# Kernel optimization log

Measured on AMD Instinct MI355X. Metric: run time of the kernel, lower is better.

The kernel has to match this reference:

```python
import jax, jax.numpy as jnp
import numpy as np

B, S, H, I, E = 2, 1024, 1024, 4096, 8

def setup_inputs() -> dict:
    key = jax.random.key(0)
    ks = jax.random.split(key, 8)
    s_h = 1.0 / np.sqrt(H)
    s_i = 1.0 / np.sqrt(I)
    return {
        "x": jax.random.normal(ks[0], (B, S, H), dtype=jnp.float32),
        "router_w": jax.random.uniform(ks[1], (H, E), jnp.float32, -s_h, s_h),
        "router_b": jax.random.uniform(ks[2], (E,), jnp.float32, -s_h, s_h),
        "w1": jax.random.uniform(ks[3], (E, H, I), jnp.float32, -s_h, s_h),
        "b1": jax.random.uniform(ks[4], (E, I), jnp.float32, -s_h, s_h),
        "w2": jax.random.uniform(ks[5], (E, I, H), jnp.float32, -s_i, s_i),
        "b2": jax.random.uniform(ks[6], (E, H), jnp.float32, -s_i, s_i),
        "game_emb": jax.random.normal(ks[7], (E, H), dtype=jnp.float32) * 0.02,
    }

def reference(x, router_w, router_b, w1, b1, w2, b2, game_emb):
    # Router: top-1 expert per token (softmax is monotone, argmax of logits)
    logits = jnp.einsum('bsh,he->bse', x, router_w) + router_b  # [B,S,E]
    expert_idx = jnp.argmax(logits, axis=-1)                    # [B,S] int
    out = jnp.zeros_like(x)
    n_experts = w1.shape[0]
    for e in range(n_experts):  # fixed small expert loop
        mask = (expert_idx == e)[..., None]                     # [B,S,1]
        sel = x + 0.1 * game_emb[e]                             # embedding add
        h = jax.nn.gelu(jnp.einsum('bsh,hi->bsi', sel, w1[e]) + b1[e], approximate=False)
        y = jnp.einsum('bsi,ih->bsh', h, w2[e]) + b2[e]
        out = jnp.where(mask, y, out)                           # scatter combine
    return out
```

## Files before the change

kernel.cpp:

```cpp
#include <hip/hip_runtime.h>
#include <hip/hip_bf16.h>
#include <math.h>

#define HDIM 1024
#define IDIM 4096
#define NE 8
#define NTOK 2048
#define PADROWS 256

typedef __attribute__((ext_vector_type(8))) short bf16x8;
typedef __attribute__((ext_vector_type(4))) float f32x4;

__device__ __forceinline__ unsigned int f2bf(float f) {
    unsigned int u = __float_as_uint(f);
    u = (u + 0x7FFFu + ((u >> 16) & 1u)) >> 16;
    return u;
}

__device__ __forceinline__ unsigned int pkbf2(float lo, float hi) {
    union { __hip_bfloat162 h; unsigned int u; } cv;
    cv.h = __float22bfloat162_rn(make_float2(lo, hi));
    return cv.u;
}

__device__ __forceinline__ float comp4(const float4& v, int c) {
    return c == 0 ? v.x : c == 1 ? v.y : c == 2 ? v.z : v.w;
}

__device__ __forceinline__ int swz8(int i) { return (i ^ (i >> 3)) & 7; }

__device__ __forceinline__ float gelu_erf(float v) {
    float x = v * 0.70710678118654752f;
    float ax = fabsf(x);
    float t = 1.0f / (1.0f + 0.3275911f * ax);
    float p = t * (0.254829592f + t * (-0.284496736f + t * (1.421413741f +
              t * (-1.453152027f + t * 1.061405429f))));
    float er = 1.0f - p * __expf(-x * x);
    er = copysignf(er, v);
    return 0.5f * v * (1.0f + er);
}

template<typename T, typename U>
__device__ __forceinline__ void gld16(const T* g, U* l) {
    __builtin_amdgcn_global_load_lds((const __attribute__((address_space(1))) void*)g,
                                     (__attribute__((address_space(3))) void*)l, 16, 0, 0);
}

__global__ __launch_bounds__(256) void router_k(const float* __restrict__ x,
                                                const float* __restrict__ rw,
                                                const float* __restrict__ rb,
                                                int* __restrict__ eidx,
                                                int* __restrict__ counts) {
    const int wave = threadIdx.x >> 6, lane = threadIdx.x & 63;
    const int t = blockIdx.x * 4 + wave;
    if (t >= NTOK) return;
    double acc[NE];
#pragma unroll
    for (int e = 0; e < NE; e++) acc[e] = 0.0;
    for (int h = lane; h < HDIM; h += 64) {
        double xv = (double)x[(size_t)t * HDIM + h];
        const float4* rwp = (const float4*)&rw[h * NE];
        float4 r0 = rwp[0], r1 = rwp[1];
        acc[0] += xv * (double)r0.x;  acc[1] += xv * (double)r0.y;
        acc[2] += xv * (double)r0.z;  acc[3] += xv * (double)r0.w;
        acc[4] += xv * (double)r1.x;  acc[5] += xv * (double)r1.y;
        acc[6] += xv * (double)r1.z;  acc[7] += xv * (double)r1.w;
    }
#pragma unroll
    for (int m = 32; m >= 1; m >>= 1) {
#pragma unroll
        for (int e = 0; e < NE; e++) acc[e] += __shfl_xor(acc[e], m);
    }
    if (lane == 0) {
        double best = acc[0] + (double)rb[0];
        int be = 0;
#pragma unroll
        for (int e = 1; e < NE; e++) {
            double v = acc[e] + (double)rb[e];
            if (v > best) { best = v; be = e; }
        }
        eidx[t] = be;
        atomicAdd(&counts[be], 1);
    }
}

__global__ void scan_k(const int* __restrict__ counts, int* __restrict__ offsets) {
    if (threadIdx.x == 0 && blockIdx.x == 0) {
        int s = 0;
        for (int e = 0; e < NE; e++) { offsets[e] = s; s += counts[e]; }
        offsets[NE] = s;
    }
}

__global__ __launch_bounds__(256) void gather_k(const float* __restrict__ x,
                                                const float* __restrict__ gemb,
                                                const int* __restrict__ eidx,
                                                const int* __restrict__ offsets,
                                                int* __restrict__ cursors,
                                                int* __restrict__ rowmap,
                                                unsigned short* __restrict__ Xg) {
    __shared__ int srow, se;
    const int t = blockIdx.x;
    if (threadIdx.x == 0) {
        int e = eidx[t];
        int pos = atomicAdd(&cursors[e], 1);
        int row = offsets[e] + pos;
        rowmap[row] = t;
        srow = row; se = e;
    }
    __syncthreads();
    const int row = srow, e = se;
    const int c = threadIdx.x * 4;
    float4 xv = *(const float4*)&x[(size_t)t * HDIM + c];
    float4 gv = *(const float4*)&gemb[(size_t)e * HDIM + c];
    ushort4 o;
    o.x = (unsigned short)f2bf(xv.x + 0.1f * gv.x);
    o.y = (unsigned short)f2bf(xv.y + 0.1f * gv.y);
    o.z = (unsigned short)f2bf(xv.z + 0.1f * gv.z);
    o.w = (unsigned short)f2bf(xv.w + 0.1f * gv.w);
    *(ushort4*)&Xg[(size_t)row * HDIM + c] = o;
}

template<int EPI>
__global__ __launch_bounds__(512, 2) void moe_gemm_k(
        const unsigned short* __restrict__ A, int lda, int Kfull, int ksplit,
        const float* __restrict__ Bw, int ldbN,
        const float* __restrict__ bias,
        const int* __restrict__ offsets, const int* __restrict__ rowmap,
        unsigned short* __restrict__ Hout, float* __restrict__ Yout,
        float* __restrict__ P, size_t pstride) {
    __shared__ __align__(16) unsigned short At[2][256 * 64];
    __shared__ __align__(16) unsigned short Bt[128 * 64];

    const int e = blockIdx.z & 7;
    const int split = blockIdx.z >> 3;
    const int rend = offsets[e + 1];
    const int r0 = offsets[e] + blockIdx.y * 256;
    if (r0 >= rend) return;
    const int c0 = blockIdx.x * 128;
    const int kbeg = split * ksplit;
    const int nt = ksplit / 64;
    const float* Be = Bw + (size_t)e * Kfull * ldbN;

    const int tid = threadIdx.x;
    const int wave = tid >> 6, lane = tid & 63;
    const int wr = (wave >> 1) * 64, wc = (wave & 1) * 64;
    const int l15 = lane & 15, l4 = lane >> 4;

    const int cg = tid & 31, kid = tid >> 5;
    const int bcol = cg * 4;
    const int boct = kid >> 1, bhalf = kid & 1;
    const float* bsrc = Be + (size_t)(kid * 4) * ldbN + c0 + bcol;
    int bwo[4];
#pragma unroll
    for (int i = 0; i < 4; ++i) {
        int col = bcol + i;
        bwo[i] = col * 64 + (boct ^ swz8(col)) * 8 + bhalf * 4;
    }

    const unsigned short* adsrc[4];
    int adoff[4];
#pragma unroll
    for (int p = 0; p < 4; ++p) {
        int gidx = p * 512 + tid;
        int row = gidx >> 3, ps = gidx & 7;
        adsrc[p] = A + (size_t)(r0 + row) * lda + (ps ^ swz8(row)) * 8;
        adoff[p] = gidx * 8;
    }

    float4 fv[4];
    auto loadB = [&](int kabs) {
#pragma unroll
        for (int j = 0; j < 4; ++j)
            fv[j] = *(const float4*)&bsrc[(size_t)(kabs + j) * ldbN];
    };
    auto dmaA = [&](int kabs, int buf) {
#pragma unroll
        for (int p = 0; p < 4; ++p)
            gld16(adsrc[p] + kabs, &At[buf][adoff[p]]);
    };

    f32x4 acc[4][4];
#pragma unroll
    for (int m = 0; m < 4; ++m)
#pragma unroll
        for (int n = 0; n < 4; ++n) acc[m][n] = (f32x4){0.f, 0.f, 0.f, 0.f};

    loadB(kbeg);
    dmaA(kbeg, 0);
    for (int t = 0; t < nt; ++t) {
        const int cur = t & 1;
#pragma unroll
        for (int i = 0; i < 4; ++i) {
            uint2 w;
            w.x = pkbf2(comp4(fv[0], i), comp4(fv[1], i));
            w.y = pkbf2(comp4(fv[2], i), comp4(fv[3], i));
            *(uint2*)&Bt[bwo[i]] = w;
        }
        if (t + 1 < nt) {
            loadB(kbeg + (t + 1) * 64);
            dmaA(kbeg + (t + 1) * 64, cur ^ 1);
            asm volatile("s_waitcnt vmcnt(8) lgkmcnt(0)" ::: "memory");
        } else {
            asm volatile("s_waitcnt vmcnt(0) lgkmcnt(0)" ::: "memory");
        }
        __builtin_amdgcn_s_barrier();
        __builtin_amdgcn_sched_barrier(0);
#pragma unroll
        for (int kh = 0; kh < 2; ++kh) {
            const int kb = kh * 4 + l4;
            bf16x8 af[4], bfr[4];
#pragma unroll
            for (int m = 0; m < 4; ++m) {
                int row = wr + m * 16 + l15;
                af[m] = *(const bf16x8*)&At[cur][row * 64 + (kb ^ swz8(row)) * 8];
            }
#pragma unroll
            for (int n = 0; n < 4; ++n) {
                int col = wc + n * 16 + l15;
                bfr[n] = *(const bf16x8*)&Bt[col * 64 + (kb ^ swz8(col)) * 8];
            }
#pragma unroll
            for (int m = 0; m < 4; ++m)
#pragma unroll
                for (int n = 0; n < 4; ++n)
                    acc[m][n] = __builtin_amdgcn_mfma_f32_16x16x32_bf16(af[m], bfr[n], acc[m][n], 0, 0, 0);
        }
        __builtin_amdgcn_sched_barrier(0);
        __builtin_amdgcn_s_barrier();
        __builtin_amdgcn_sched_barrier(0);
    }

#pragma unroll
    for (int m = 0; m < 4; ++m) {
#pragma unroll
        for (int r = 0; r < 4; ++r) {
            const int row = r0 + wr + m * 16 + l4 * 4 + r;
            if (row < rend) {
                if constexpr (EPI == 0) {
#pragma unroll
                    for (int n = 0; n < 4; ++n) {
                        int col = c0 + wc + n * 16 + l15;
                        float v = acc[m][n][r] + bias[(size_t)e * ldbN + col];
                        Hout[(size_t)row * IDIM + col] = (unsigned short)f2bf(gelu_erf(v));
                    }
                } else if (split == 0) {
                    const int tt = rowmap[row];
#pragma unroll
                    for (int n = 0; n < 4; ++n) {
                        int col = c0 + wc + n * 16 + l15;
                        Yout[(size_t)tt * HDIM + col] = acc[m][n][r] + bias[(size_t)e * ldbN + col];
                    }
                } else {
                    float* Ps = P + (size_t)(split - 1) * pstride;
#pragma unroll
                    for (int n = 0; n < 4; ++n) {
                        int col = c0 + wc + n * 16 + l15;
                        Ps[(size_t)row * HDIM + col] = acc[m][n][r];
                    }
                }
            }
        }
    }
}

__global__ __launch_bounds__(256) void reduce_k(const float* __restrict__ P,
                                                size_t pstride, int nparts,
                                                const int* __restrict__ rowmap,
                                                float* __restrict__ out) {
    const int row = blockIdx.x;
    const int t = rowmap[row];
    const int c = threadIdx.x * 4;
    f32x4 s = *(const f32x4*)&out[(size_t)t * HDIM + c];
    for (int p = 0; p < nparts; ++p)
        s += *(const f32x4*)&P[(size_t)p * pstride + (size_t)row * HDIM + c];
    *(f32x4*)&out[(size_t)t * HDIM + c] = s;
}

extern "C" void kernel_launch(void* const* d_in, const int* in_sizes, int n_in,
                              void* d_out, int out_size, void* d_ws, size_t ws_size,
                              hipStream_t stream) {
    const float* x    = (const float*)d_in[0];
    const float* rw   = (const float*)d_in[1];
    const float* rb   = (const float*)d_in[2];
    const float* w1   = (const float*)d_in[3];
    const float* b1   = (const float*)d_in[4];
    const float* w2   = (const float*)d_in[5];
    const float* b2   = (const float*)d_in[6];
    const float* gemb = (const float*)d_in[7];
    float* out = (float*)d_out;

    char* ws = (char*)d_ws;
    int* meta    = (int*)ws;
    int* counts  = meta;
    int* cursors = meta + 8;
    int* offsets = meta + 16;
    int* eidx    = meta + 32;
    int* rowmap  = meta + 32 + NTOK;
    size_t off = 32768;
    unsigned short* Xg = (unsigned short*)(ws + off);
    off += (size_t)(NTOK + PADROWS) * HDIM * 2;
    unsigned short* Hbuf = (unsigned short*)(ws + off);
    off += (size_t)(NTOK + PADROWS) * IDIM * 2;
    float* P = (float*)(ws + off);
    const size_t pstride = (size_t)NTOK * HDIM;
    int nsplit = 1;
    if (ws_size >= off + 3 * pstride * 4) nsplit = 4;
    else if (ws_size >= off + 1 * pstride * 4) nsplit = 2;

    hipMemsetAsync(counts, 0, 16 * sizeof(int), stream);
    router_k<<<NTOK / 4, 256, 0, stream>>>(x, rw, rb, eidx, counts);
    scan_k<<<1, 64, 0, stream>>>(counts, offsets);
    gather_k<<<NTOK, 256, 0, stream>>>(x, gemb, eidx, offsets, cursors, rowmap, Xg);
    moe_gemm_k<0><<<dim3(IDIM / 128, 3, NE), 512, 0, stream>>>(
        Xg, HDIM, HDIM, HDIM, w1, IDIM, b1, offsets, rowmap, Hbuf, nullptr, nullptr, 0);
    moe_gemm_k<1><<<dim3(HDIM / 128, 3, NE * nsplit), 512, 0, stream>>>(
        Hbuf, IDIM, IDIM, IDIM / nsplit, w2, HDIM, b2, offsets, rowmap, nullptr, out, P, pstride);
    if (nsplit > 1)
        reduce_k<<<NTOK, 256, 0, stream>>>(P, pstride, nsplit - 1, rowmap, out);
}
```

Before: 228.3 us.

## Retile expert GEMM to 1024-thread blocks with double-buffered B, single A

```diff
diff --git a/kernel.cpp b/kernel.cpp
--- a/kernel.cpp
+++ b/kernel.cpp
@@ -122,85 +122,88 @@
 }
 
 template<int EPI>
-__global__ __launch_bounds__(512, 2) void moe_gemm_k(
+__global__ __launch_bounds__(1024, 4) void moe_gemm_k(
         const unsigned short* __restrict__ A, int lda, int Kfull, int ksplit,
         const float* __restrict__ Bw, int ldbN,
         const float* __restrict__ bias,
         const int* __restrict__ offsets, const int* __restrict__ rowmap,
         unsigned short* __restrict__ Hout, float* __restrict__ Yout,
-        float* __restrict__ P, size_t pstride) {
-    __shared__ __align__(16) unsigned short At[2][256 * 64];
-    __shared__ __align__(16) unsigned short Bt[128 * 64];
-
-    const int e = blockIdx.z & 7;
-    const int split = blockIdx.z >> 3;
+        float* __restrict__ P, size_t pstride, int ncb, int nsp) {
+    __shared__ __align__(16) unsigned short At[256 * 64];
+    __shared__ __align__(16) unsigned short Bt[2][128 * 64];
+
+    const int bid = blockIdx.x;
+    const int e = bid & 7;
+    int loc = bid >> 3;
+    const int cblk = loc % ncb;  loc /= ncb;
+    const int split = loc % nsp;
+    const int yblk = loc / nsp;
+
     const int rend = offsets[e + 1];
-    const int r0 = offsets[e] + blockIdx.y * 256;
+    const int r0 = offsets[e] + yblk * 256;
     if (r0 >= rend) return;
-    const int c0 = blockIdx.x * 128;
+    const int c0 = cblk * 128;
     const int kbeg = split * ksplit;
     const int nt = ksplit / 64;
     const float* Be = Bw + (size_t)e * Kfull * ldbN;
 
     const int tid = threadIdx.x;
     const int wave = tid >> 6, lane = tid & 63;
-    const int wr = (wave >> 1) * 64, wc = (wave & 1) * 64;
+    const int wr = (wave >> 2) * 64;
+    const int wc = (wave & 3) * 32;
     const int l15 = lane & 15, l4 = lane >> 4;
 
     const int cg = tid & 31, kid = tid >> 5;
     const int bcol = cg * 4;
-    const int boct = kid >> 1, bhalf = kid & 1;
-    const float* bsrc = Be + (size_t)(kid * 4) * ldbN + c0 + bcol;
+    const int boct = kid >> 2;
+    const int brow = (kid * 2) & 7;
+    const float* bsrc = Be + (size_t)(kid * 2) * ldbN + c0 + bcol;
     int bwo[4];
 #pragma unroll
     for (int i = 0; i < 4; ++i) {
         int col = bcol + i;
-        bwo[i] = col * 64 + (boct ^ swz8(col)) * 8 + bhalf * 4;
-    }
-
-    const unsigned short* adsrc[4];
-    int adoff[4];
-#pragma unroll
-    for (int p = 0; p < 4; ++p) {
-        int gidx = p * 512 + tid;
+        bwo[i] = col * 64 + (boct ^ swz8(col)) * 8 + brow;
+    }
+
+    const unsigned short* adsrc[2];
+    int adoff[2];
+#pragma unroll
+    for (int p = 0; p < 2; ++p) {
+        int gidx = p * 1024 + tid;
         int row = gidx >> 3, ps = gidx & 7;
         adsrc[p] = A + (size_t)(r0 + row) * lda + (ps ^ swz8(row)) * 8;
         adoff[p] = gidx * 8;
     }
 
-    float4 fv[4];
+    float4 fv[2];
     auto loadB = [&](int kabs) {
 #pragma unroll
-        for (int j = 0; j < 4; ++j)
+        for (int j = 0; j < 2; ++j)
             fv[j] = *(const float4*)&bsrc[(size_t)(kabs + j) * ldbN];
     };
-    auto dmaA = [&](int kabs, int buf) {
-#pragma unroll
-        for (int p = 0; p < 4; ++p)
-            gld16(adsrc[p] + kabs, &At[buf][adoff[p]]);
+    auto dmaA = [&](int kabs) {
+#pragma unroll
+        for (int p = 0; p < 2; ++p)
+            gld16(adsrc[p] + kabs, &At[adoff[p]]);
     };
 
-    f32x4 acc[4][4];
+    f32x4 acc[4][2];
 #pragma unroll
     for (int m = 0; m < 4; ++m)
 #pragma unroll
-        for (int n = 0; n < 4; ++n) acc[m][n] = (f32x4){0.f, 0.f, 0.f, 0.f};
+        for (int n = 0; n < 2; ++n) acc[m][n] = (f32x4){0.f, 0.f, 0.f, 0.f};
 
     loadB(kbeg);
-    dmaA(kbeg, 0);
+    dmaA(kbeg);
     for (int t = 0; t < nt; ++t) {
         const int cur = t & 1;
-#pragma unroll
-        for (int i = 0; i < 4; ++i) {
-            uint2 w;
-            w.x = pkbf2(comp4(fv[0], i), comp4(fv[1], i));
-            w.y = pkbf2(comp4(fv[2], i), comp4(fv[3], i));
-            *(uint2*)&Bt[bwo[i]] = w;
-        }
+        if (t > 0) dmaA(kbeg + t * 64);
+#pragma unroll
+        for (int i = 0; i < 4; ++i)
+            *(unsigned int*)&Bt[cur][bwo[i]] = pkbf2(comp4(fv[0], i), comp4(fv[1], i));
         if (t + 1 < nt) {
             loadB(kbeg + (t + 1) * 64);
-            dmaA(kbeg + (t + 1) * 64, cur ^ 1);
-            asm volatile("s_waitcnt vmcnt(8) lgkmcnt(0)" ::: "memory");
+            asm volatile("s_waitcnt vmcnt(2) lgkmcnt(0)" ::: "memory");
         } else {
             asm volatile("s_waitcnt vmcnt(0) lgkmcnt(0)" ::: "memory");
         }
@@ -209,21 +212,21 @@
 #pragma unroll
         for (int kh = 0; kh < 2; ++kh) {
             const int kb = kh * 4 + l4;
-            bf16x8 af[4], bfr[4];
+            bf16x8 af[4], bfr[2];
 #pragma unroll
             for (int m = 0; m < 4; ++m) {
                 int row = wr + m * 16 + l15;
-                af[m] = *(const bf16x8*)&At[cur][row * 64 + (kb ^ swz8(row)) * 8];
+                af[m] = *(const bf16x8*)&At[row * 64 + (kb ^ swz8(row)) * 8];
             }
 #pragma unroll
-            for (int n = 0; n < 4; ++n) {
+            for (int n = 0; n < 2; ++n) {
                 int col = wc + n * 16 + l15;
-                bfr[n] = *(const bf16x8*)&Bt[col * 64 + (kb ^ swz8(col)) * 8];
+                bfr[n] = *(const bf16x8*)&Bt[cur][col * 64 + (kb ^ swz8(col)) * 8];
             }
 #pragma unroll
             for (int m = 0; m < 4; ++m)
 #pragma unroll
-                for (int n = 0; n < 4; ++n)
+                for (int n = 0; n < 2; ++n)
                     acc[m][n] = __builtin_amdgcn_mfma_f32_16x16x32_bf16(af[m], bfr[n], acc[m][n], 0, 0, 0);
         }
         __builtin_amdgcn_sched_barrier(0);
@@ -239,7 +242,7 @@
             if (row < rend) {
                 if constexpr (EPI == 0) {
 #pragma unroll
-                    for (int n = 0; n < 4; ++n) {
+                    for (int n = 0; n < 2; ++n) {
                         int col = c0 + wc + n * 16 + l15;
                         float v = acc[m][n][r] + bias[(size_t)e * ldbN + col];
                         Hout[(size_t)row * IDIM + col] = (unsigned short)f2bf(gelu_erf(v));
@@ -247,14 +250,14 @@
                 } else if (split == 0) {
                     const int tt = rowmap[row];
 #pragma unroll
-                    for (int n = 0; n < 4; ++n) {
+                    for (int n = 0; n < 2; ++n) {
                         int col = c0 + wc + n * 16 + l15;
                         Yout[(size_t)tt * HDIM + col] = acc[m][n][r] + bias[(size_t)e * ldbN + col];
                     }
                 } else {
                     float* Ps = P + (size_t)(split - 1) * pstride;
 #pragma unroll
-                    for (int n = 0; n < 4; ++n) {
+                    for (int n = 0; n < 2; ++n) {
                         int col = c0 + wc + n * 16 + l15;
                         Ps[(size_t)row * HDIM + col] = acc[m][n][r];
                     }
@@ -312,10 +315,12 @@
     router_k<<<NTOK / 4, 256, 0, stream>>>(x, rw, rb, eidx, counts);
     scan_k<<<1, 64, 0, stream>>>(counts, offsets);
     gather_k<<<NTOK, 256, 0, stream>>>(x, gemb, eidx, offsets, cursors, rowmap, Xg);
-    moe_gemm_k<0><<<dim3(IDIM / 128, 3, NE), 512, 0, stream>>>(
-        Xg, HDIM, HDIM, HDIM, w1, IDIM, b1, offsets, rowmap, Hbuf, nullptr, nullptr, 0);
-    moe_gemm_k<1><<<dim3(HDIM / 128, 3, NE * nsplit), 512, 0, stream>>>(
-        Hbuf, IDIM, IDIM, IDIM / nsplit, w2, HDIM, b2, offsets, rowmap, nullptr, out, P, pstride);
+    moe_gemm_k<0><<<512, 1024, 0, stream>>>(
+        Xg, HDIM, HDIM, HDIM, w1, IDIM, b1, offsets, rowmap,
+        Hbuf, nullptr, nullptr, 0, 32, 1);
+    moe_gemm_k<1><<<128 * nsplit, 1024, 0, stream>>>(
+        Hbuf, IDIM, IDIM, IDIM / nsplit, w2, HDIM, b2, offsets, rowmap,
+        nullptr, out, P, pstride, 8, nsplit);
     if (nsplit > 1)
         reduce_k<<<NTOK, 256, 0, stream>>>(P, pstride, nsplit - 1, rowmap, out);
 }
```

New measurement: 210.0 us. 8.0% less time.

## Split-K the first MoE GEMM with a fused GELU combine; flatten and interleave grids

Applied to the files above, without the earlier changes.

```diff
diff --git a/kernel.cpp b/kernel.cpp
--- a/kernel.cpp
+++ b/kernel.cpp
@@ -122,40 +122,47 @@
 }
 
 template<int EPI>
-__global__ __launch_bounds__(512, 2) void moe_gemm_k(
+__global__ __launch_bounds__(512, 4) void moe_gemm_k(
         const unsigned short* __restrict__ A, int lda, int Kfull, int ksplit,
         const float* __restrict__ Bw, int ldbN,
         const float* __restrict__ bias,
         const int* __restrict__ offsets, const int* __restrict__ rowmap,
         unsigned short* __restrict__ Hout, float* __restrict__ Yout,
-        float* __restrict__ P, size_t pstride) {
+        float* __restrict__ Pdst, size_t pstride, int ncb, int nsp) {
     __shared__ __align__(16) unsigned short At[2][256 * 64];
     __shared__ __align__(16) unsigned short Bt[128 * 64];
 
-    const int e = blockIdx.z & 7;
-    const int split = blockIdx.z >> 3;
+    const int bid = blockIdx.x;
+    const int e = bid & 7;
+    int loc = bid >> 3;
+    const int cblk = loc % ncb;  loc /= ncb;
+    const int split = loc % nsp;
+    const int yblk = loc / nsp;
+
     const int rend = offsets[e + 1];
-    const int r0 = offsets[e] + blockIdx.y * 256;
+    const int r0 = offsets[e] + yblk * 256;
     if (r0 >= rend) return;
-    const int c0 = blockIdx.x * 128;
+    const int c0 = cblk * 128;
     const int kbeg = split * ksplit;
     const int nt = ksplit / 64;
     const float* Be = Bw + (size_t)e * Kfull * ldbN;
 
     const int tid = threadIdx.x;
     const int wave = tid >> 6, lane = tid & 63;
-    const int wr = (wave >> 1) * 64, wc = (wave & 1) * 64;
+    const int wr = (wave >> 1) * 64;
+    const int wc = (wave & 1) * 64;
     const int l15 = lane & 15, l4 = lane >> 4;
 
-    const int cg = tid & 31, kid = tid >> 5;
+    const int cg = tid & 31, kg = tid >> 5;
     const int bcol = cg * 4;
-    const int boct = kid >> 1, bhalf = kid & 1;
-    const float* bsrc = Be + (size_t)(kid * 4) * ldbN + c0 + bcol;
+    const int boct = kg >> 1;
+    const int bpos = (kg * 4) & 7;
+    const float* bsrc = Be + (size_t)(kg * 4) * ldbN + c0 + bcol;
     int bwo[4];
 #pragma unroll
     for (int i = 0; i < 4; ++i) {
         int col = bcol + i;
-        bwo[i] = col * 64 + (boct ^ swz8(col)) * 8 + bhalf * 4;
+        bwo[i] = col * 64 + ((boct ^ swz8(col)) << 3) + bpos;
     }
 
     const unsigned short* adsrc[4];
@@ -237,14 +244,14 @@
         for (int r = 0; r < 4; ++r) {
             const int row = r0 + wr + m * 16 + l4 * 4 + r;
             if (row < rend) {
-                if constexpr (EPI == 0) {
+                if constexpr (EPI == 2) {
 #pragma unroll
                     for (int n = 0; n < 4; ++n) {
                         int col = c0 + wc + n * 16 + l15;
                         float v = acc[m][n][r] + bias[(size_t)e * ldbN + col];
                         Hout[(size_t)row * IDIM + col] = (unsigned short)f2bf(gelu_erf(v));
                     }
-                } else if (split == 0) {
+                } else if (EPI == 1 && split == 0) {
                     const int tt = rowmap[row];
 #pragma unroll
                     for (int n = 0; n < 4; ++n) {
@@ -252,15 +259,42 @@
                         Yout[(size_t)tt * HDIM + col] = acc[m][n][r] + bias[(size_t)e * ldbN + col];
                     }
                 } else {
-                    float* Ps = P + (size_t)(split - 1) * pstride;
+                    const int slot = (EPI == 1) ? split - 1 : split;
+                    float* Ps = Pdst + (size_t)slot * pstride;
 #pragma unroll
                     for (int n = 0; n < 4; ++n) {
                         int col = c0 + wc + n * 16 + l15;
-                        Ps[(size_t)row * HDIM + col] = acc[m][n][r];
+                        Ps[(size_t)row * ldbN + col] = acc[m][n][r];
                     }
                 }
             }
         }
+    }
+}
+
+__global__ __launch_bounds__(256) void gelu_combine_k(const float* __restrict__ H0,
+                                                      const float* __restrict__ P1,
+                                                      const float* __restrict__ b1,
+                                                      const int* __restrict__ offsets,
+                                                      unsigned short* __restrict__ Hbuf) {
+    const int row = blockIdx.x;
+    int e = 0;
+#pragma unroll
+    for (int i = 1; i < NE; ++i) e += (row >= offsets[i]);
+    const float* bp = b1 + (size_t)e * IDIM;
+    const size_t base = (size_t)row * IDIM;
+#pragma unroll
+    for (int it = 0; it < 4; ++it) {
+        int c = it * 1024 + threadIdx.x * 4;
+        f32x4 a = *(const f32x4*)&H0[base + c];
+        f32x4 b = *(const f32x4*)&P1[base + c];
+        f32x4 bb = *(const f32x4*)&bp[c];
+        ushort4 o;
+        o.x = (unsigned short)f2bf(gelu_erf(a[0] + b[0] + bb[0]));
+        o.y = (unsigned short)f2bf(gelu_erf(a[1] + b[1] + bb[1]));
+        o.z = (unsigned short)f2bf(gelu_erf(a[2] + b[2] + bb[2]));
+        o.w = (unsigned short)f2bf(gelu_erf(a[3] + b[3] + bb[3]));
+        *(ushort4*)&Hbuf[base + c] = o;
     }
 }
 
@@ -302,20 +336,39 @@
     off += (size_t)(NTOK + PADROWS) * HDIM * 2;
     unsigned short* Hbuf = (unsigned short*)(ws + off);
     off += (size_t)(NTOK + PADROWS) * IDIM * 2;
-    float* P = (float*)(ws + off);
-    const size_t pstride = (size_t)NTOK * HDIM;
-    int nsplit = 1;
-    if (ws_size >= off + 3 * pstride * 4) nsplit = 4;
-    else if (ws_size >= off + 1 * pstride * 4) nsplit = 2;
+
+    const size_t f1elems = (size_t)NTOK * IDIM;
+    float* Hraw = nullptr;
+    if (ws_size >= off + 2 * f1elems * 4) {
+        Hraw = (float*)(ws + off);
+        off += 2 * f1elems * 4;
+    }
+    float* P2 = (float*)(ws + off);
+    const size_t ps2 = (size_t)NTOK * HDIM;
+    size_t rem = (ws_size > off) ? ws_size - off : 0;
+    int nsp2 = 1;
+    if (rem >= 7 * ps2 * 4) nsp2 = 8;
+    else if (rem >= 3 * ps2 * 4) nsp2 = 4;
+    else if (rem >= 1 * ps2 * 4) nsp2 = 2;
 
     hipMemsetAsync(counts, 0, 16 * sizeof(int), stream);
     router_k<<<NTOK / 4, 256, 0, stream>>>(x, rw, rb, eidx, counts);
     scan_k<<<1, 64, 0, stream>>>(counts, offsets);
     gather_k<<<NTOK, 256, 0, stream>>>(x, gemb, eidx, offsets, cursors, rowmap, Xg);
-    moe_gemm_k<0><<<dim3(IDIM / 128, 3, NE), 512, 0, stream>>>(
-        Xg, HDIM, HDIM, HDIM, w1, IDIM, b1, offsets, rowmap, Hbuf, nullptr, nullptr, 0);
-    moe_gemm_k<1><<<dim3(HDIM / 128, 3, NE * nsplit), 512, 0, stream>>>(
-        Hbuf, IDIM, IDIM, IDIM / nsplit, w2, HDIM, b2, offsets, rowmap, nullptr, out, P, pstride);
-    if (nsplit > 1)
-        reduce_k<<<NTOK, 256, 0, stream>>>(P, pstride, nsplit - 1, rowmap, out);
-}
+
+    if (Hraw) {
+        moe_gemm_k<0><<<8 * 32 * 2 * 2, 512, 0, stream>>>(
+            Xg, HDIM, HDIM, HDIM / 2, w1, IDIM, b1, offsets, rowmap,
+            nullptr, nullptr, Hraw, f1elems, 32, 2);
+        gelu_combine_k<<<NTOK, 256, 0, stream>>>(Hraw, Hraw + f1elems, b1, offsets, Hbuf);
+    } else {
+        moe_gemm_k<2><<<8 * 32 * 1 * 2, 512, 0, stream>>>(
+            Xg, HDIM, HDIM, HDIM, w1, IDIM, b1, offsets, rowmap,
+            Hbuf, nullptr, nullptr, 0, 32, 1);
+    }
+    moe_gemm_k<1><<<8 * 8 * nsp2 * 2, 512, 0, stream>>>(
+        Hbuf, IDIM, IDIM, IDIM / nsp2, w2, HDIM, b2, offsets, rowmap,
+        nullptr, out, P2, ps2, 8, nsp2);
+    if (nsp2 > 1)
+        reduce_k<<<NTOK, 256, 0, stream>>>(P2, ps2, nsp2 - 1, rowmap, out);
+}
```

Result: slower. 336.3 us (+47.3%).
